# Kernel tuning notes

Hardware: AMD Instinct MI355X
Metric: run time of the kernel (lower is better)

Reference implementation:

```python
import jax, jax.numpy as jnp
import numpy as np

B, N, D, E = 2, 50000, 128, 640000


def setup_inputs() -> dict:
    key = jax.random.key(0)
    ks = jax.random.split(key, 7)
    x = jax.random.normal(ks[0], (B, N, D), dtype=jnp.float32)
    edge_index = jax.random.randint(ks[1], (2, E), 0, N)
    edge_attr = jax.random.uniform(ks[2], (E,), dtype=jnp.float32)
    s = 1.0 / np.sqrt(D)
    W1 = jax.random.uniform(ks[3], (D, D), jnp.float32, -s, s)
    b1 = jax.random.uniform(ks[4], (D,), jnp.float32, -s, s)
    W2 = jax.random.uniform(ks[5], (D, D), jnp.float32, -s, s)
    b2 = jax.random.uniform(ks[6], (D,), jnp.float32, -s, s)
    return {"x": x, "edge_index": edge_index, "edge_attr": edge_attr,
            "W1": W1, "b1": b1, "W2": W2, "b2": b2}


def _gcn_layer(x, W, b, row, col, norm, n):
    # x: [B, N, D] -> transform then gather-scale-scatter along edges
    h = jnp.einsum('bnd,df->bnf', x, W)
    msg = h[:, row, :] * norm[None, :, None]          # [B, E2, D]
    agg = jax.vmap(lambda m: jax.ops.segment_sum(m, col, num_segments=n))(msg)
    return agg + b


def reference(x, edge_index, edge_attr, W1, b1, W2, b2):
    n = x.shape[1]
    row, col = edge_index[0], edge_index[1]
    # GCNConv default: add self loops (weight 1), symmetric normalization
    loop = jnp.arange(n)
    row2 = jnp.concatenate([row, loop])
    col2 = jnp.concatenate([col, loop])
    w2 = jnp.concatenate([edge_attr, jnp.ones((n,), edge_attr.dtype)])
    deg = jax.ops.segment_sum(w2, col2, num_segments=n)
    dinv = jnp.where(deg > 0, jax.lax.rsqrt(deg), 0.0)
    norm = dinv[row2] * w2 * dinv[col2]               # [E2]
    # dropout is identity in eval mode
    h = jax.nn.relu(_gcn_layer(x, W1, b1, row2, col2, norm, n))
    h = jax.nn.relu(_gcn_layer(h, W2, b2, row2, col2, norm, n))
    return h
```

## Files before the change

### kernel.cpp

```cpp
#include <hip/hip_runtime.h>

#define NNODES 50000
#define NBATCH 2
#define DIM    128
#define NEDGE  640000
#define M_TOT  (NBATCH*NNODES)
#define NXCD   8
#define NBL_N  196
#define NBL_GB 6250

typedef unsigned short u16;
typedef unsigned int   u32;
typedef unsigned long long u64;

typedef __attribute__((ext_vector_type(8))) short bf16x8;
typedef __attribute__((ext_vector_type(4))) float f32x4;

__device__ __forceinline__ float bf2f(u16 u){ return __uint_as_float(((u32)u)<<16); }
__device__ __forceinline__ u16 f2bf(float f){
    u32 x = __float_as_uint(f);
    x += 0x7fffu + ((x>>16)&1u);
    return (u16)(x>>16);
}

__global__ __launch_bounds__(256) void count_k(const int* __restrict__ ei,
                                               const float* __restrict__ ea,
                                               u64* __restrict__ part,
                                               u32* __restrict__ rankpack){
    u32 xcc = __builtin_amdgcn_s_getreg(6164) & 7u;
    int e = blockIdx.x*256 + threadIdx.x;
    if (e < NEDGE){
        int c = ei[NEDGE + e];
        u64 inc = (((u64)__float2uint_rn(ea[e] * 16777216.0f)) << 32) | 1ull;
        u64 old = __hip_atomic_fetch_add(&part[(size_t)xcc*NNODES + c], inc,
                                         __ATOMIC_RELAXED, __HIP_MEMORY_SCOPE_WORKGROUP);
        rankpack[e] = ((u32)old & 0xffffu) | (xcc << 16);
    }
}

__global__ __launch_bounds__(256) void scan1(const u64* __restrict__ part,
                                             int* __restrict__ cnt,
                                             int* __restrict__ poff,
                                             float* __restrict__ dinv,
                                             int* colstart, int* bsum){
    __shared__ int s[256];
    int tid = threadIdx.x;
    int n = blockIdx.x*256 + tid;
    int v = 0;
    if (n < NNODES){
        int run = 0; u64 fsum = 0;
        #pragma unroll
        for (int p = 0; p < NXCD; ++p){
            u64 pv = part[(size_t)p*NNODES + n];
            poff[p*NNODES + n] = run;
            run  += (int)(pv & 0xffffffffu);
            fsum += (pv >> 32);
        }
        cnt[n] = run;
        v = run;
        float deg = 1.0f + (float)fsum * (1.0f/16777216.0f);
        dinv[n] = rsqrtf(deg);
    }
    s[tid] = v; __syncthreads();
    #pragma unroll
    for (int off = 1; off < 256; off <<= 1){
        int t = (tid >= off) ? s[tid-off] : 0;
        __syncthreads();
        s[tid] += t;
        __syncthreads();
    }
    if (n < NNODES) colstart[n] = s[tid] - v;
    if (tid == 255) bsum[blockIdx.x] = s[255];
}

__global__ __launch_bounds__(256) void fill_k(const int* __restrict__ ei,
                                              const float* __restrict__ ea,
                                              const float* __restrict__ dinv,
                                              const int* __restrict__ colstart,
                                              const int* __restrict__ bsum,
                                              const int* __restrict__ poff,
                                              const u32* __restrict__ rankpack,
                                              int* __restrict__ colstartF,
                                              u32* __restrict__ epk){
    __shared__ int s[256];
    __shared__ int pre[256];
    int tid = threadIdx.x;
    int v = (tid < NBL_N) ? bsum[tid] : 0;
    s[tid] = v; __syncthreads();
    #pragma unroll
    for (int off = 1; off < 256; off <<= 1){
        int t = (tid >= off) ? s[tid-off] : 0;
        __syncthreads();
        s[tid] += t;
        __syncthreads();
    }
    pre[tid] = s[tid] - v;
    __syncthreads();

    int e = blockIdx.x*256 + tid;
    if (e < NEDGE){
        int r = ei[e], c = ei[NEDGE + e];
        u32 rp = rankpack[e];
        int base = colstart[c] + pre[c >> 8];
        colstartF[c] = base;
        int pos = base + poff[(rp >> 16)*NNODES + c] + (int)(rp & 0xffffu);
        float w = dinv[r] * ea[e] * dinv[c];
        epk[pos] = (u32)r | ((u32)f2bf(w) << 16);
    }
}

__global__ __launch_bounds__(256) void transposeW(const float* __restrict__ W1, u16* __restrict__ Wt1,
                                                  const float* __restrict__ W2, u16* __restrict__ Wt2,
                                                  u64* __restrict__ part){
    int i = blockIdx.x*256 + threadIdx.x;
    const float* W = (i < 16384) ? W1 : W2;
    u16* Wt       = (i < 16384) ? Wt1 : Wt2;
    int ii = i & 16383;
    int k = ii >> 7, n = ii & 127;
    Wt[n*DIM + k] = f2bf(W[ii]);
    for (int z = i; z < NXCD*NNODES; z += 32768) part[z] = 0;
}

__device__ __forceinline__ bf16x8 load_frag(const float* A, size_t off){
    const f32x4* ap = (const f32x4*)(A + off);
    f32x4 lo = __builtin_nontemporal_load(ap);
    f32x4 hi = __builtin_nontemporal_load(ap + 1);
    bf16x8 r;
    r[0] = (short)f2bf(lo.x); r[1] = (short)f2bf(lo.y);
    r[2] = (short)f2bf(lo.z); r[3] = (short)f2bf(lo.w);
    r[4] = (short)f2bf(hi.x); r[5] = (short)f2bf(hi.y);
    r[6] = (short)f2bf(hi.z); r[7] = (short)f2bf(hi.w);
    return r;
}
__device__ __forceinline__ bf16x8 load_frag(const u16* A, size_t off){
    return *(const bf16x8*)(A + off);
}

template <typename AT>
__global__ __launch_bounds__(256, 4) void gemm128(const AT* __restrict__ A,
                                                  const u16* __restrict__ Wt,
                                                  u16* __restrict__ H, int M){
    __shared__ u16 Wl[128][136];
    int tid = threadIdx.x;
    {
        const uint4* src = (const uint4*)Wt;
        #pragma unroll
        for (int j = 0; j < 8; ++j){
            int g = tid + j*256;
            *(uint4*)&Wl[g >> 4][(g & 15)*8] = src[g];
        }
    }
    __syncthreads();

    int wave = tid >> 6, lane = tid & 63;
    int quad = lane >> 4, r = lane & 15;
    int row0 = blockIdx.x*128;
    int rbase = row0 + wave*32;

    f32x4 acc[2][8];
    #pragma unroll
    for (int mt = 0; mt < 2; ++mt)
        #pragma unroll
        for (int nt = 0; nt < 8; ++nt)
            acc[mt][nt] = (f32x4){0.f,0.f,0.f,0.f};

    #pragma unroll
    for (int ks = 0; ks < 4; ++ks){
        bf16x8 af[2];
        #pragma unroll
        for (int mt = 0; mt < 2; ++mt){
            int row = rbase + mt*16 + r;
            if (row < M)
                af[mt] = load_frag(A, (size_t)row*DIM + ks*32 + quad*8);
            else
                af[mt] = (bf16x8){0,0,0,0,0,0,0,0};
        }
        #pragma unroll
        for (int nt = 0; nt < 8; ++nt){
            bf16x8 bfr = *(const bf16x8*)&Wl[nt*16 + r][ks*32 + quad*8];
            #pragma unroll
            for (int mt = 0; mt < 2; ++mt)
                acc[mt][nt] = __builtin_amdgcn_mfma_f32_16x16x32_bf16(af[mt], bfr, acc[mt][nt], 0, 0, 0);
        }
    }

    __syncthreads();
    #pragma unroll
    for (int mt = 0; mt < 2; ++mt)
        #pragma unroll
        for (int nt = 0; nt < 8; ++nt)
            #pragma unroll
            for (int reg = 0; reg < 4; ++reg)
                Wl[wave*32 + mt*16 + quad*4 + reg][nt*16 + r] = f2bf(acc[mt][nt][reg]);
    __syncthreads();

    #pragma unroll
    for (int j = 0; j < 8; ++j){
        int g = tid + j*256;
        int rl = g >> 4, ch = g & 15;
        int row = row0 + rl;
        if (row < M)
            *(uint4*)((char*)H + (size_t)row*256 + ch*16) = *(const uint4*)&Wl[rl][ch*8];
    }
}

template <bool OUT_F32>
__global__ __launch_bounds__(256) void gather8_k(const u16* __restrict__ H,
                                                 const u32* __restrict__ epk,
                                                 const int* __restrict__ colstartF,
                                                 const int* __restrict__ cnt,
                                                 const float* __restrict__ dinv,
                                                 const float* __restrict__ bias,
                                                 void* __restrict__ out){
    int wave = threadIdx.x >> 6, lane = threadIdx.x & 63;
    int sub = lane & 31, half = lane >> 5;
    int bid = blockIdx.x;
    int b   = (bid >= NBL_GB);
    int n   = (bid - b*NBL_GB)*8 + wave*2 + half;
    const char* Hb = (const char*)(H + (size_t)b*NNODES*DIM);

    float a0, a1, a2, a3;
    {
        uint2 sv = *(const uint2*)(Hb + (size_t)n*256 + sub*8);
        float dn = dinv[n], dn2 = dn*dn;
        a0 = dn2*__uint_as_float(sv.x << 16);
        a1 = dn2*__uint_as_float(sv.x & 0xffff0000u);
        a2 = dn2*__uint_as_float(sv.y << 16);
        a3 = dn2*__uint_as_float(sv.y & 0xffff0000u);
    }

    int s = colstartF[n], c = cnt[n];
    for (int base = 0; base < c; base += 32){
        int m = min(32, c - base);
        u32 em = 0;
        if (sub < m) em = epk[s + base + sub];
        for (int j = 0; j < m; j += 8){
            #pragma unroll
            for (int g = 0; g < 8; ++g){
                u32 me = __shfl(em, half*32 + j + g);
                uint2 v = *(const uint2*)(Hb + (size_t)(me & 0xffffu)*256 + sub*8);
                float w = __uint_as_float(me & 0xffff0000u);
                a0 = fmaf(w, __uint_as_float(v.x << 16), a0);
                a1 = fmaf(w, __uint_as_float(v.x & 0xffff0000u), a1);
                a2 = fmaf(w, __uint_as_float(v.y << 16), a2);
                a3 = fmaf(w, __uint_as_float(v.y & 0xffff0000u), a3);
            }
        }
    }

    float4 bb = ((const float4*)bias)[sub];
    a0 = fmaxf(a0 + bb.x, 0.f);
    a1 = fmaxf(a1 + bb.y, 0.f);
    a2 = fmaxf(a2 + bb.z, 0.f);
    a3 = fmaxf(a3 + bb.w, 0.f);
    if (OUT_F32){
        float* O = (float*)out + ((size_t)b*NNODES + n)*DIM + sub*4;
        *(float4*)O = make_float4(a0, a1, a2, a3);
    } else {
        char* O = (char*)out + ((size_t)b*NNODES + n)*256 + sub*8;
        uint2 pk;
        pk.x = (u32)f2bf(a0) | ((u32)f2bf(a1) << 16);
        pk.y = (u32)f2bf(a2) | ((u32)f2bf(a3) << 16);
        *(uint2*)O = pk;
    }
}

extern "C" void kernel_launch(void* const* d_in, const int* in_sizes, int n_in,
                              void* d_out, int out_size, void* d_ws, size_t ws_size,
                              hipStream_t stream){
    const float* x  = (const float*)d_in[0];
    const int*   ei = (const int*)  d_in[1];
    const float* ea = (const float*)d_in[2];
    const float* W1 = (const float*)d_in[3];
    const float* b1 = (const float*)d_in[4];
    const float* W2 = (const float*)d_in[5];
    const float* b2 = (const float*)d_in[6];

    char* p = (char*)d_ws;
    auto alloc = [&](size_t bytes)->char*{ char* r = p; p += (bytes + 511) & ~(size_t)511; return r; };
    u64*   part     = (u64*)  alloc((size_t)NXCD*NNODES*8);
    u32*   rankpack = (u32*)  alloc((size_t)NEDGE*4);
    int*   poff     = (int*)  alloc((size_t)NXCD*NNODES*4);
    float* dinv     = (float*)alloc(NNODES*4);
    int*   cnt      = (int*)  alloc(NNODES*4);
    int*   colstart = (int*)  alloc(NNODES*4);
    int*   colstartF= (int*)  alloc(NNODES*4);
    int*   bsum     = (int*)  alloc(1024);
    u32*   epk      = (u32*)  alloc((size_t)NEDGE*4);
    u16*   Wt1      = (u16*)  alloc(DIM*DIM*2);
    u16*   Wt2      = (u16*)  alloc(DIM*DIM*2);
    u16*   h        = (u16*)  alloc((size_t)M_TOT*DIM*2);
    u16*   o1       = (u16*)  alloc((size_t)M_TOT*DIM*2);

    const int NBL_E = (NEDGE  + 255)/256;
    const int NTILE = (M_TOT + 127)/128;
    const int NBL_G = 2*NBL_GB;

    transposeW<<<128, 256, 0, stream>>>(W1, Wt1, W2, Wt2, part);
    count_k<<<NBL_E, 256, 0, stream>>>(ei, ea, part, rankpack);
    scan1  <<<NBL_N, 256, 0, stream>>>(part, cnt, poff, dinv, colstart, bsum);
    fill_k <<<NBL_E, 256, 0, stream>>>(ei, ea, dinv, colstart, bsum, poff, rankpack, colstartF, epk);

    gemm128<float><<<NTILE, 256, 0, stream>>>(x,  Wt1, h, M_TOT);
    gather8_k<false><<<NBL_G, 256, 0, stream>>>(h,  epk, colstartF, cnt, dinv, b1, o1);
    gemm128<u16  ><<<NTILE, 256, 0, stream>>>(o1, Wt2, h, M_TOT);
    gather8_k<true ><<<NBL_G, 256, 0, stream>>>(h,  epk, colstartF, cnt, dinv, b2, d_out);
}
```

Baseline: 278.1 us.

## Fold weight transpose into count kernel, memset partials, split GEMM/gather per batch

Removes the separate transposeW kernel: the zeroing of the per-XCD partial counts becomes a hipMemsetAsync, and the weight transpose/bf16 conversion runs as extra blocks appended to count_k. The GEMM and gather launches are each split into two launches, one per batch half, with the batch index passed as a parameter. This trims one kernel launch and the index arithmetic in the gather. In exchange it adds several extra launches whose boundaries serialize on the stream, and smaller grids may tail worse.

```diff
diff --git a/kernel.cpp b/kernel.cpp
--- a/kernel.cpp
+++ b/kernel.cpp
@@ -7,6 +7,7 @@
 #define M_TOT  (NBATCH*NNODES)
 #define NXCD   8
 #define NBL_N  196
+#define NBL_E  2500
 #define NBL_GB 6250
 
 typedef unsigned short u16;
@@ -26,15 +27,25 @@
 __global__ __launch_bounds__(256) void count_k(const int* __restrict__ ei,
                                                const float* __restrict__ ea,
                                                u64* __restrict__ part,
-                                               u32* __restrict__ rankpack){
-    u32 xcc = __builtin_amdgcn_s_getreg(6164) & 7u;
-    int e = blockIdx.x*256 + threadIdx.x;
-    if (e < NEDGE){
+                                               u32* __restrict__ rankpack,
+                                               const float* __restrict__ W1, u16* __restrict__ Wt1,
+                                               const float* __restrict__ W2, u16* __restrict__ Wt2){
+    int bid = blockIdx.x;
+    if (bid < NBL_E){
+        u32 xcc = __builtin_amdgcn_s_getreg(6164) & 7u;
+        int e = bid*256 + threadIdx.x;
         int c = ei[NEDGE + e];
         u64 inc = (((u64)__float2uint_rn(ea[e] * 16777216.0f)) << 32) | 1ull;
         u64 old = __hip_atomic_fetch_add(&part[(size_t)xcc*NNODES + c], inc,
                                          __ATOMIC_RELAXED, __HIP_MEMORY_SCOPE_WORKGROUP);
         rankpack[e] = ((u32)old & 0xffffu) | (xcc << 16);
+    } else {
+        int i = (bid - NBL_E)*256 + threadIdx.x;
+        const float* W = (i < 16384) ? W1 : W2;
+        u16* Wt       = (i < 16384) ? Wt1 : Wt2;
+        int ii = i & 16383;
+        int k = ii >> 7, n = ii & 127;
+        Wt[n*DIM + k] = f2bf(W[ii]);
     }
 }
 
@@ -109,18 +120,6 @@
     }
 }
 
-__global__ __launch_bounds__(256) void transposeW(const float* __restrict__ W1, u16* __restrict__ Wt1,
-                                                  const float* __restrict__ W2, u16* __restrict__ Wt2,
-                                                  u64* __restrict__ part){
-    int i = blockIdx.x*256 + threadIdx.x;
-    const float* W = (i < 16384) ? W1 : W2;
-    u16* Wt       = (i < 16384) ? Wt1 : Wt2;
-    int ii = i & 16383;
-    int k = ii >> 7, n = ii & 127;
-    Wt[n*DIM + k] = f2bf(W[ii]);
-    for (int z = i; z < NXCD*NNODES; z += 32768) part[z] = 0;
-}
-
 __device__ __forceinline__ bf16x8 load_frag(const float* A, size_t off){
     const f32x4* ap = (const f32x4*)(A + off);
     f32x4 lo = __builtin_nontemporal_load(ap);
@@ -139,7 +138,8 @@
 template <typename AT>
 __global__ __launch_bounds__(256, 4) void gemm128(const AT* __restrict__ A,
                                                   const u16* __restrict__ Wt,
-                                                  u16* __restrict__ H, int M){
+                                                  u16* __restrict__ H, int M,
+                                                  int tile_base){
     __shared__ u16 Wl[128][136];
     int tid = threadIdx.x;
     {
@@ -154,7 +154,7 @@
 
     int wave = tid >> 6, lane = tid & 63;
     int quad = lane >> 4, r = lane & 15;
-    int row0 = blockIdx.x*128;
+    int row0 = (tile_base + blockIdx.x)*128;
     int rbase = row0 + wave*32;
 
     f32x4 acc[2][8];
@@ -211,12 +211,10 @@
                                                  const int* __restrict__ cnt,
                                                  const float* __restrict__ dinv,
                                                  const float* __restrict__ bias,
-                                                 void* __restrict__ out){
+                                                 void* __restrict__ out, int b){
     int wave = threadIdx.x >> 6, lane = threadIdx.x & 63;
     int sub = lane & 31, half = lane >> 5;
-    int bid = blockIdx.x;
-    int b   = (bid >= NBL_GB);
-    int n   = (bid - b*NBL_GB)*8 + wave*2 + half;
+    int n   = blockIdx.x*8 + wave*2 + half;
     const char* Hb = (const char*)(H + (size_t)b*NNODES*DIM);
 
     float a0, a1, a2, a3;
@@ -292,17 +290,20 @@
     u16*   h        = (u16*)  alloc((size_t)M_TOT*DIM*2);
     u16*   o1       = (u16*)  alloc((size_t)M_TOT*DIM*2);
 
-    const int NBL_E = (NEDGE  + 255)/256;
-    const int NTILE = (M_TOT + 127)/128;
-    const int NBL_G = 2*NBL_GB;
-
-    transposeW<<<128, 256, 0, stream>>>(W1, Wt1, W2, Wt2, part);
-    count_k<<<NBL_E, 256, 0, stream>>>(ei, ea, part, rankpack);
+    const int NTILE  = (M_TOT + 127)/128;
+    const int NTILE_H = NTILE/2;
+
+    hipMemsetAsync(part, 0, (size_t)NXCD*NNODES*8, stream);
+    count_k<<<NBL_E + 128, 256, 0, stream>>>(ei, ea, part, rankpack, W1, Wt1, W2, Wt2);
     scan1  <<<NBL_N, 256, 0, stream>>>(part, cnt, poff, dinv, colstart, bsum);
     fill_k <<<NBL_E, 256, 0, stream>>>(ei, ea, dinv, colstart, bsum, poff, rankpack, colstartF, epk);
 
-    gemm128<float><<<NTILE, 256, 0, stream>>>(x,  Wt1, h, M_TOT);
-    gather8_k<false><<<NBL_G, 256, 0, stream>>>(h,  epk, colstartF, cnt, dinv, b1, o1);
-    gemm128<u16  ><<<NTILE, 256, 0, stream>>>(o1, Wt2, h, M_TOT);
-    gather8_k<true ><<<NBL_G, 256, 0, stream>>>(h,  epk, colstartF, cnt, dinv, b2, d_out);
-}
+    gemm128<float><<<NTILE_H, 256, 0, stream>>>(x,  Wt1, h, M_TOT, 0);
+    gemm128<float><<<NTILE_H, 256, 0, stream>>>(x,  Wt1, h, M_TOT, NTILE_H);
+    gather8_k<false><<<NBL_GB, 256, 0, stream>>>(h,  epk, colstartF, cnt, dinv, b1, o1, 0);
+    gather8_k<false><<<NBL_GB, 256, 0, stream>>>(h,  epk, colstartF, cnt, dinv, b1, o1, 1);
+    gemm128<u16  ><<<NTILE_H, 256, 0, stream>>>(o1, Wt2, h, M_TOT, 0);
+    gemm128<u16  ><<<NTILE_H, 256, 0, stream>>>(o1, Wt2, h, M_TOT, NTILE_H);
+    gather8_k<true ><<<NBL_GB, 256, 0, stream>>>(h,  epk, colstartF, cnt, dinv, b2, d_out, 0);
+    gather8_k<true ><<<NBL_GB, 256, 0, stream>>>(h,  epk, colstartF, cnt, dinv, b2, d_out, 1);
+}
```

New measurement: 297.0 us. 6.8% more time.

## Fuse second-layer GEMM into first gather kernel via shuffle-based per-node matvec

Applied to the files above, without the earlier changes.

The first aggregation kernel now also applies the second layer's weight matrix. W2 is loaded into shared memory and each half-wave does a 128x128 matvec with FMA and lane shuffles, writing H2 directly. This removes the separate second GEMM launch and the round trip of the intermediate o1 through memory. In exchange, a tensor-core MFMA GEMM is replaced by scalar FMAs (about 16K FMAs per node), and each 512-thread block uses 32KB of LDS, which may reduce occupancy for the latency-bound gather.

```diff
diff --git a/kernel.cpp b/kernel.cpp
--- a/kernel.cpp
+++ b/kernel.cpp
@@ -8,6 +8,7 @@
 #define NXCD   8
 #define NBL_N  196
 #define NBL_GB 6250
+#define NBL_FB 3125
 
 typedef unsigned short u16;
 typedef unsigned int   u32;
@@ -110,14 +111,16 @@
 }
 
 __global__ __launch_bounds__(256) void transposeW(const float* __restrict__ W1, u16* __restrict__ Wt1,
-                                                  const float* __restrict__ W2, u16* __restrict__ Wt2,
+                                                  const float* __restrict__ W2, u16* __restrict__ Wb2,
                                                   u64* __restrict__ part){
     int i = blockIdx.x*256 + threadIdx.x;
-    const float* W = (i < 16384) ? W1 : W2;
-    u16* Wt       = (i < 16384) ? Wt1 : Wt2;
-    int ii = i & 16383;
-    int k = ii >> 7, n = ii & 127;
-    Wt[n*DIM + k] = f2bf(W[ii]);
+    if (i < 16384){
+        int k = i >> 7, n = i & 127;
+        Wt1[n*DIM + k] = f2bf(W1[i]);
+    } else {
+        int ii = i & 16383;
+        Wb2[ii] = f2bf(W2[ii]);
+    }
     for (int z = i; z < NXCD*NNODES; z += 32768) part[z] = 0;
 }
 
@@ -132,12 +135,8 @@
     r[6] = (short)f2bf(hi.z); r[7] = (short)f2bf(hi.w);
     return r;
 }
-__device__ __forceinline__ bf16x8 load_frag(const u16* A, size_t off){
-    return *(const bf16x8*)(A + off);
-}
-
-template <typename AT>
-__global__ __launch_bounds__(256, 4) void gemm128(const AT* __restrict__ A,
+
+__global__ __launch_bounds__(256, 4) void gemm1_k(const float* __restrict__ A,
                                                   const u16* __restrict__ Wt,
                                                   u16* __restrict__ H, int M){
     __shared__ u16 Wl[128][136];
@@ -204,19 +203,31 @@
     }
 }
 
-template <bool OUT_F32>
-__global__ __launch_bounds__(256) void gather8_k(const u16* __restrict__ H,
+__global__ __launch_bounds__(512) void gatherF_k(const u16* __restrict__ H,
                                                  const u32* __restrict__ epk,
                                                  const int* __restrict__ colstartF,
                                                  const int* __restrict__ cnt,
                                                  const float* __restrict__ dinv,
                                                  const float* __restrict__ bias,
-                                                 void* __restrict__ out){
-    int wave = threadIdx.x >> 6, lane = threadIdx.x & 63;
+                                                 const u16* __restrict__ Wb2,
+                                                 u16* __restrict__ H2){
+    __shared__ u16 W2l[128*128];
+    int tid = threadIdx.x;
+    {
+        const uint4* src = (const uint4*)Wb2;
+        #pragma unroll
+        for (int j = 0; j < 4; ++j){
+            int g = tid + j*512;
+            *(uint4*)&W2l[g*8] = src[g];
+        }
+    }
+    __syncthreads();
+
+    int bid = blockIdx.x;
+    int b   = (bid >= NBL_FB);
+    int wid = tid >> 6, lane = tid & 63;
     int sub = lane & 31, half = lane >> 5;
-    int bid = blockIdx.x;
-    int b   = (bid >= NBL_GB);
-    int n   = (bid - b*NBL_GB)*8 + wave*2 + half;
+    int n   = (bid - b*NBL_FB)*16 + wid*2 + half;
     const char* Hb = (const char*)(H + (size_t)b*NNODES*DIM);
 
     float a0, a1, a2, a3;
@@ -248,21 +259,102 @@
         }
     }
 
+    {
+        float4 bb = ((const float4*)bias)[sub];
+        a0 = fmaxf(a0 + bb.x, 0.f);
+        a1 = fmaxf(a1 + bb.y, 0.f);
+        a2 = fmaxf(a2 + bb.z, 0.f);
+        a3 = fmaxf(a3 + bb.w, 0.f);
+    }
+
+    float h0 = 0.f, h1 = 0.f, h2 = 0.f, h3 = 0.f;
+    #pragma unroll 4
+    for (int kk = 0; kk < 32; ++kk){
+        int srcl = half*32 + kk;
+        float w0 = __shfl(a0, srcl);
+        float w1 = __shfl(a1, srcl);
+        float w2 = __shfl(a2, srcl);
+        float w3 = __shfl(a3, srcl);
+        const u16* Wr = &W2l[(4*kk)*128 + 4*sub];
+        uint2 v0 = *(const uint2*)(Wr);
+        uint2 v1 = *(const uint2*)(Wr + 128);
+        uint2 v2 = *(const uint2*)(Wr + 256);
+        uint2 v3 = *(const uint2*)(Wr + 384);
+        h0 = fmaf(w0, __uint_as_float(v0.x << 16), h0);
+        h1 = fmaf(w0, __uint_as_float(v0.x & 0xffff0000u), h1);
+        h2 = fmaf(w0, __uint_as_float(v0.y << 16), h2);
+        h3 = fmaf(w0, __uint_as_float(v0.y & 0xffff0000u), h3);
+        h0 = fmaf(w1, __uint_as_float(v1.x << 16), h0);
+        h1 = fmaf(w1, __uint_as_float(v1.x & 0xffff0000u), h1);
+        h2 = fmaf(w1, __uint_as_float(v1.y << 16), h2);
+        h3 = fmaf(w1, __uint_as_float(v1.y & 0xffff0000u), h3);
+        h0 = fmaf(w2, __uint_as_float(v2.x << 16), h0);
+        h1 = fmaf(w2, __uint_as_float(v2.x & 0xffff0000u), h1);
+        h2 = fmaf(w2, __uint_as_float(v2.y << 16), h2);
+        h3 = fmaf(w2, __uint_as_float(v2.y & 0xffff0000u), h3);
+        h0 = fmaf(w3, __uint_as_float(v3.x << 16), h0);
+        h1 = fmaf(w3, __uint_as_float(v3.x & 0xffff0000u), h1);
+        h2 = fmaf(w3, __uint_as_float(v3.y << 16), h2);
+        h3 = fmaf(w3, __uint_as_float(v3.y & 0xffff0000u), h3);
+    }
+
+    char* O = (char*)H2 + ((size_t)b*NNODES + n)*256 + sub*8;
+    uint2 pk;
+    pk.x = (u32)f2bf(h0) | ((u32)f2bf(h1) << 16);
+    pk.y = (u32)f2bf(h2) | ((u32)f2bf(h3) << 16);
+    *(uint2*)O = pk;
+}
+
+__global__ __launch_bounds__(256) void gather8_k(const u16* __restrict__ H,
+                                                 const u32* __restrict__ epk,
+                                                 const int* __restrict__ colstartF,
+                                                 const int* __restrict__ cnt,
+                                                 const float* __restrict__ dinv,
+                                                 const float* __restrict__ bias,
+                                                 float* __restrict__ out){
+    int wave = threadIdx.x >> 6, lane = threadIdx.x & 63;
+    int sub = lane & 31, half = lane >> 5;
+    int bid = blockIdx.x;
+    int b   = (bid >= NBL_GB);
+    int n   = (bid - b*NBL_GB)*8 + wave*2 + half;
+    const char* Hb = (const char*)(H + (size_t)b*NNODES*DIM);
+
+    float a0, a1, a2, a3;
+    {
+        uint2 sv = *(const uint2*)(Hb + (size_t)n*256 + sub*8);
+        float dn = dinv[n], dn2 = dn*dn;
+        a0 = dn2*__uint_as_float(sv.x << 16);
+        a1 = dn2*__uint_as_float(sv.x & 0xffff0000u);
+        a2 = dn2*__uint_as_float(sv.y << 16);
+        a3 = dn2*__uint_as_float(sv.y & 0xffff0000u);
+    }
+
+    int s = colstartF[n], c = cnt[n];
+    for (int base = 0; base < c; base += 32){
+        int m = min(32, c - base);
+        u32 em = 0;
+        if (sub < m) em = epk[s + base + sub];
+        for (int j = 0; j < m; j += 8){
+            #pragma unroll
+            for (int g = 0; g < 8; ++g){
+                u32 me = __shfl(em, half*32 + j + g);
+                uint2 v = *(const uint2*)(Hb + (size_t)(me & 0xffffu)*256 + sub*8);
+                float w = __uint_as_float(me & 0xffff0000u);
+                a0 = fmaf(w, __uint_as_float(v.x << 16), a0);
+                a1 = fmaf(w, __uint_as_float(v.x & 0xffff0000u), a1);
+                a2 = fmaf(w, __uint_as_float(v.y << 16), a2);
+                a3 = fmaf(w, __uint_as_float(v.y & 0xffff0000u), a3);
+            }
+        }
+    }
+
     float4 bb = ((const float4*)bias)[sub];
     a0 = fmaxf(a0 + bb.x, 0.f);
     a1 = fmaxf(a1 + bb.y, 0.f);
     a2 = fmaxf(a2 + bb.z, 0.f);
     a3 = fmaxf(a3 + bb.w, 0.f);
-    if (OUT_F32){
-        float* O = (float*)out + ((size_t)b*NNODES + n)*DIM + sub*4;
-        *(float4*)O = make_float4(a0, a1, a2, a3);
-    } else {
-        char* O = (char*)out + ((size_t)b*NNODES + n)*256 + sub*8;
-        uint2 pk;
-        pk.x = (u32)f2bf(a0) | ((u32)f2bf(a1) << 16);
-        pk.y = (u32)f2bf(a2) | ((u32)f2bf(a3) << 16);
-        *(uint2*)O = pk;
-    }
+    float* O = out + ((size_t)b*NNODES + n)*DIM + sub*4;
+    *(float4*)O = make_float4(a0, a1, a2, a3);
 }
 
 extern "C" void kernel_launch(void* const* d_in, const int* in_sizes, int n_in,
@@ -288,21 +380,19 @@
     int*   bsum     = (int*)  alloc(1024);
     u32*   epk      = (u32*)  alloc((size_t)NEDGE*4);
     u16*   Wt1      = (u16*)  alloc(DIM*DIM*2);
-    u16*   Wt2      = (u16*)  alloc(DIM*DIM*2);
+    u16*   Wb2      = (u16*)  alloc(DIM*DIM*2);
     u16*   h        = (u16*)  alloc((size_t)M_TOT*DIM*2);
-    u16*   o1       = (u16*)  alloc((size_t)M_TOT*DIM*2);
+    u16*   h2       = (u16*)  alloc((size_t)M_TOT*DIM*2);
 
     const int NBL_E = (NEDGE  + 255)/256;
     const int NTILE = (M_TOT + 127)/128;
-    const int NBL_G = 2*NBL_GB;
-
-    transposeW<<<128, 256, 0, stream>>>(W1, Wt1, W2, Wt2, part);
+
+    transposeW<<<128, 256, 0, stream>>>(W1, Wt1, W2, Wb2, part);
     count_k<<<NBL_E, 256, 0, stream>>>(ei, ea, part, rankpack);
     scan1  <<<NBL_N, 256, 0, stream>>>(part, cnt, poff, dinv, colstart, bsum);
     fill_k <<<NBL_E, 256, 0, stream>>>(ei, ea, dinv, colstart, bsum, poff, rankpack, colstartF, epk);
 
-    gemm128<float><<<NTILE, 256, 0, stream>>>(x,  Wt1, h, M_TOT);
-    gather8_k<false><<<NBL_G, 256, 0, stream>>>(h,  epk, colstartF, cnt, dinv, b1, o1);
-    gemm128<u16  ><<<NTILE, 256, 0, stream>>>(o1, Wt2, h, M_TOT);
-    gather8_k<true ><<<NBL_G, 256, 0, stream>>>(h,  epk, colstartF, cnt, dinv, b2, d_out);
-}
+    gemm1_k<<<NTILE, 256, 0, stream>>>(x, Wt1, h, M_TOT);
+    gatherF_k<<<2*NBL_FB, 512, 0, stream>>>(h, epk, colstartF, cnt, dinv, b1, Wb2, h2);
+    gather8_k<<<2*NBL_GB, 256, 0, stream>>>(h2, epk, colstartF, cnt, dinv, b2, (float*)d_out);
+}
```

Measured after the change: 348.6 us. 25.4% more time.
